# Kernel optimization log

Hardware: AMD Instinct MI355X
Metric: run time of the kernel (lower is better)

## Reference

```python
import jax, jax.numpy as jnp
import numpy as np

B, T, H = 32, 2000, 512      # batch, encoder frames, d_model
L = 256                      # max label length (padded output tokens)
THRESHOLD = 0.95


def setup_inputs() -> dict:
    key = jax.random.key(0)
    k1, k2, k3 = jax.random.split(key, 3)
    hidden = jax.random.normal(k1, (B, T, H), dtype=jnp.float32)
    alphas = jax.random.uniform(k2, (B, T), dtype=jnp.float32)
    target_lengths = jax.random.randint(k3, (B,), 64, L + 1)
    return {"hidden": hidden, "alphas": alphas, "target_lengths": target_lengths}


def _cif(hidden, alphas):
    # Continuous integrate-and-fire scan over time.
    Bt, Tt, Ht = hidden.shape

    def step(carry, xs):
        integrate, frame = carry          # [B], [B,H]
        alpha, h = xs                     # [B], [B,H]
        dist_completion = 1.0 - integrate
        integrate = integrate + alpha
        fire = integrate >= THRESHOLD     # [B] bool
        cur = jnp.where(fire, dist_completion, alpha)
        remainds = alpha - cur
        frame_out = frame + cur[:, None] * h
        integ_next = jnp.where(fire, integrate - 1.0, integrate)
        frame_next = jnp.where(fire[:, None], remainds[:, None] * h, frame_out)
        return (integ_next, frame_next), (frame_out, fire)

    init = (jnp.zeros((Bt,), hidden.dtype), jnp.zeros((Bt, Ht), hidden.dtype))
    _, (frames, fires) = jax.lax.scan(step, init, (alphas.T, jnp.swapaxes(hidden, 0, 1)))
    frames = jnp.swapaxes(frames, 0, 1)   # [B,T,H] accumulated frame at each step
    fires = fires.T                        # [B,T] fire events

    # Gather fired frames into padded [B, L, H] token tensor (vectorized scatter).
    tok = jnp.cumsum(fires.astype(jnp.int32), axis=1) - 1   # token index per fired frame
    valid = fires & (tok >= 0) & (tok < L)
    out = jnp.zeros((Bt, L, Ht), hidden.dtype)
    b_idx = jnp.arange(Bt)[:, None]
    out = out.at[b_idx, jnp.clip(tok, 0, L - 1)].add(
        frames * valid[..., None].astype(hidden.dtype))
    return out


def reference(hidden, alphas, target_lengths):
    # Rescale alphas so each row sums to target length (noise term omitted).
    num = target_lengths.astype(alphas.dtype)
    alphas = alphas * (num / alphas.sum(-1))[:, None]
    return _cif(hidden, alphas)
```

## Files before the change

kernel.cpp:

```cpp
#include <hip/hip_runtime.h>

#define BB 32
#define TT 2000
#define NG 500
#define NW 63
#define HH 512
#define LL 256
#define THRESH 0.95f


__global__ __launch_bounds__(256) void cif_scan_kernel(
    const float* __restrict__ alphas, const int* __restrict__ tlen,
    int2* __restrict__ rec, int* __restrict__ nfires,
    float* __restrict__ scale_g)
{
    const int b = blockIdx.x;
    const int tid = threadIdx.x;
    __shared__ float sa[TT];
    __shared__ float sinteg[TT];
    __shared__ double red[256];
    __shared__ unsigned smask[NW];
    __shared__ int spre[NW + 1];
    __shared__ float s_scale;

    const float4* a4 = (const float4*)(alphas + b * TT);
    float4* sa4 = (float4*)sa;
    double s = 0.0;
    for (int g = tid; g < NG; g += 256) {
        float4 v = a4[g];
        sa4[g] = v;
        s += (double)v.x + (double)v.y + (double)v.z + (double)v.w;
    }
    red[tid] = s;
    __syncthreads();
    for (int off = 128; off > 0; off >>= 1) {
        if (tid < off) red[tid] += red[tid + off];
        __syncthreads();
    }
    if (tid == 0) {
        const float sumf = (float)red[0];
        const float sc = (float)tlen[b] / sumf;
        s_scale = sc;
        scale_g[b] = sc;
    }
    __syncthreads();
    const float sc = s_scale;

    for (int g = tid; g < NG; g += 256) {
        float4 v = sa4[g];
        v.x *= sc; v.y *= sc; v.z *= sc; v.w *= sc;
        sa4[g] = v;
    }
    __syncthreads();

    if (tid == 0) {
        const float4* s4 = (const float4*)sa;
        float4* ip4 = (float4*)sinteg;
        float integ = 0.0f;
        unsigned mask = 0;
        float4 buf[8];
        #pragma unroll
        for (int i = 0; i < 8; ++i) buf[i] = s4[i];

        for (int w = 0; w < 62; ++w) {
            #pragma unroll
            for (int i = 0; i < 8; ++i) {
                const int g = w * 8 + i;
                const float4 c = buf[i];
                if (g + 8 < NG) buf[i] = s4[g + 8];
                const float av[4] = {c.x, c.y, c.z, c.w};
                float iv[4];
                #pragma unroll
                for (int j = 0; j < 4; ++j) {
                    const float a = av[j];
                    float ii = integ + a;
                    const bool fire = (ii >= THRESH);
                    const float iim1 = ii - 1.0f;
                    ii = fire ? iim1 : ii;
                    mask |= fire ? (1u << (i * 4 + j)) : 0u;
                    iv[j] = ii;
                    integ = ii;
                }
                ip4[g] = make_float4(iv[0], iv[1], iv[2], iv[3]);
            }
            smask[w] = mask;
            mask = 0;
        }
        #pragma unroll
        for (int i = 0; i < 4; ++i) {
            const int g = 496 + i;
            const float4 c = buf[i];
            const float av[4] = {c.x, c.y, c.z, c.w};
            float iv[4];
            #pragma unroll
            for (int j = 0; j < 4; ++j) {
                const float a = av[j];
                float ii = integ + a;
                const bool fire = (ii >= THRESH);
                const float iim1 = ii - 1.0f;
                ii = fire ? iim1 : ii;
                mask |= fire ? (1u << (i * 4 + j)) : 0u;
                iv[j] = ii;
                integ = ii;
            }
            ip4[g] = make_float4(iv[0], iv[1], iv[2], iv[3]);
        }
        smask[62] = mask;
    }
    __syncthreads();

    if (tid == 0) {
        int r = 0;
        for (int w = 0; w < NW; ++w) { spre[w] = r; r += __popc(smask[w]); }
        spre[NW] = r;
        nfires[b] = (r < LL) ? r : LL;
    }
    __syncthreads();
    if (tid < NW) {
        unsigned m = smask[tid];
        int tok = spre[tid];
        while (m) {
            const int j = __ffs(m) - 1;
            m &= m - 1;
            const int t = tid * 32 + j;
            if (tok < LL) {
                const float dist = (t == 0) ? 1.0f : (1.0f - sinteg[t - 1]);
                int2 r; r.x = t; r.y = __float_as_int(dist);
                rec[b * LL + tok] = r;
            }
            ++tok;
        }
    }
}

__global__ __launch_bounds__(128) void cif_gather_kernel(
    const float* __restrict__ hidden, const float* __restrict__ alphas,
    const float* __restrict__ scale_g, const int2* __restrict__ rec,
    const int* __restrict__ nfires, float* __restrict__ out)
{
    const int l = blockIdx.x;
    const int b = blockIdx.y;
    const int tid = threadIdx.x;

    float4 acc = make_float4(0.f, 0.f, 0.f, 0.f);
    const int F = nfires[b];
    if (l < F) {
        const int2 re = rec[b * LL + l];
        const int e = re.x;
        const float dist = __int_as_float(re.y);
        const float sc = scale_g[b];
        const float* hb = hidden + (size_t)b * TT * HH + (size_t)tid * 4;
        const float* ab = alphas + b * TT;
        int t0 = 0;
        if (l > 0) {
            const int2 rp = rec[b * LL + l - 1];
            const int sp = rp.x;
            const float dp = __int_as_float(rp.y);
            const float rem = ab[sp] * sc - dp;
            const float4 hv = *(const float4*)(hb + (size_t)sp * HH);
            acc.x = rem * hv.x; acc.y = rem * hv.y;
            acc.z = rem * hv.z; acc.w = rem * hv.w;
            t0 = sp + 1;
        }
        int t = t0;
        float w0 = (t < e) ? ab[t] * sc : dist;
        float4 h0 = *(const float4*)(hb + (size_t)t * HH);
        if (t < e) {
            float w1 = (t + 1 < e) ? ab[t + 1] * sc : dist;
            float4 h1 = *(const float4*)(hb + (size_t)(t + 1) * HH);
            while (t + 2 <= e) {
                const float w2 = (t + 2 < e) ? ab[t + 2] * sc : dist;
                const float4 h2 = *(const float4*)(hb + (size_t)(t + 2) * HH);
                acc.x += w0 * h0.x; acc.y += w0 * h0.y;
                acc.z += w0 * h0.z; acc.w += w0 * h0.w;
                w0 = w1; h0 = h1; w1 = w2; h1 = h2; ++t;
            }
            acc.x += w0 * h0.x; acc.y += w0 * h0.y;
            acc.z += w0 * h0.z; acc.w += w0 * h0.w;
            w0 = w1; h0 = h1;
        }
        acc.x += w0 * h0.x; acc.y += w0 * h0.y;
        acc.z += w0 * h0.z; acc.w += w0 * h0.w;
    }
    *(float4*)(out + ((size_t)b * LL + l) * HH + (size_t)tid * 4) = acc;
}

extern "C" void kernel_launch(void* const* d_in, const int* in_sizes, int n_in,
                              void* d_out, int out_size, void* d_ws, size_t ws_size,
                              hipStream_t stream) {
    const float* hidden = (const float*)d_in[0];
    const float* alphas = (const float*)d_in[1];
    const int*   tlen   = (const int*)d_in[2];
    float* out = (float*)d_out;

    int2*  rec     = (int2*)d_ws;
    int*   nfires  = (int*)(rec + BB * LL);
    float* scale_g = (float*)(nfires + BB);

    cif_scan_kernel<<<BB, 256, 0, stream>>>(alphas, tlen, rec, nfires, scale_g);
    cif_gather_kernel<<<dim3(LL, BB), 128, 0, stream>>>(hidden, alphas, scale_g,
                                                        rec, nfires, out);
}
```

Measured before the change: 264.6 us.

## Split scale reduction and batch eight rows per scan block with chunked transposed staging

Moves the alpha-sum reduction into its own kernel and turns the scan into 4 blocks, each handling 8 batch rows. Each block streams alphas in 512-frame chunks into a padded transposed shared buffer, and 8 threads scan their rows in parallel. Firing records are emitted serially per row with a carried token counter. This lowers the scan's block count and adds an extra launch, trading occupancy for shared staging. The serial per-thread record emission may lengthen the critical path.

```diff
diff --git a/kernel.cpp b/kernel.cpp
--- a/kernel.cpp
+++ b/kernel.cpp
@@ -3,32 +3,28 @@
 #define BB 32
 #define TT 2000
 #define NG 500
-#define NW 63
 #define HH 512
 #define LL 256
 #define THRESH 0.95f
 
+#define CHUNK 512
+#define NCH 4
+#define BPB 8
+#define SPAD 9
+#define NWIN 16
 
-__global__ __launch_bounds__(256) void cif_scan_kernel(
+
+__global__ __launch_bounds__(256) void cif_scale_kernel(
     const float* __restrict__ alphas, const int* __restrict__ tlen,
-    int2* __restrict__ rec, int* __restrict__ nfires,
     float* __restrict__ scale_g)
 {
     const int b = blockIdx.x;
     const int tid = threadIdx.x;
-    __shared__ float sa[TT];
-    __shared__ float sinteg[TT];
     __shared__ double red[256];
-    __shared__ unsigned smask[NW];
-    __shared__ int spre[NW + 1];
-    __shared__ float s_scale;
-
     const float4* a4 = (const float4*)(alphas + b * TT);
-    float4* sa4 = (float4*)sa;
     double s = 0.0;
     for (int g = tid; g < NG; g += 256) {
         float4 v = a4[g];
-        sa4[g] = v;
         s += (double)v.x + (double)v.y + (double)v.z + (double)v.w;
     }
     red[tid] = s;
@@ -37,100 +33,88 @@
         if (tid < off) red[tid] += red[tid + off];
         __syncthreads();
     }
-    if (tid == 0) {
-        const float sumf = (float)red[0];
-        const float sc = (float)tlen[b] / sumf;
-        s_scale = sc;
-        scale_g[b] = sc;
-    }
-    __syncthreads();
-    const float sc = s_scale;
+    if (tid == 0)
+        scale_g[b] = (float)tlen[b] / (float)red[0];
+}
 
-    for (int g = tid; g < NG; g += 256) {
-        float4 v = sa4[g];
-        v.x *= sc; v.y *= sc; v.z *= sc; v.w *= sc;
-        sa4[g] = v;
-    }
+__global__ __launch_bounds__(256) void cif_scan_kernel(
+    const float* __restrict__ alphas, const float* __restrict__ scale_g,
+    int2* __restrict__ rec, int* __restrict__ nfires)
+{
+    const int b0 = blockIdx.x * BPB;
+    const int tid = threadIdx.x;
+    __shared__ float saT[CHUNK * SPAD];
+    __shared__ float ipT[CHUNK * SPAD];
+    __shared__ unsigned smask[NWIN * BPB];
+    __shared__ float scs[BPB];
+
+    if (tid < BPB) scs[tid] = scale_g[b0 + tid];
     __syncthreads();
 
-    if (tid == 0) {
-        const float4* s4 = (const float4*)sa;
-        float4* ip4 = (float4*)sinteg;
-        float integ = 0.0f;
-        unsigned mask = 0;
-        float4 buf[8];
-        #pragma unroll
-        for (int i = 0; i < 8; ++i) buf[i] = s4[i];
+    float integ = 0.0f;
+    float carry_in = 0.0f;
+    int tok = 0;
 
-        for (int w = 0; w < 62; ++w) {
+    for (int c = 0; c < NCH; ++c) {
+        {
+            const int bl = tid >> 5;
+            const int lane = tid & 31;
+            const float sc = scs[bl];
+            const float* arow = alphas + (size_t)(b0 + bl) * TT + c * CHUNK;
             #pragma unroll
-            for (int i = 0; i < 8; ++i) {
-                const int g = w * 8 + i;
-                const float4 c = buf[i];
-                if (g + 8 < NG) buf[i] = s4[g + 8];
-                const float av[4] = {c.x, c.y, c.z, c.w};
-                float iv[4];
+            for (int j = 0; j < CHUNK / 32; ++j) {
+                const int t = lane + j * 32;
+                const int gt = c * CHUNK + t;
+                const float a = (gt < TT) ? arow[t] : 0.0f;
+                saT[t * SPAD + bl] = a * sc;
+            }
+        }
+        __syncthreads();
+
+        if (tid < BPB) {
+            carry_in = integ;
+            for (int w = 0; w < NWIN; ++w) {
+                unsigned mask = 0;
                 #pragma unroll
-                for (int j = 0; j < 4; ++j) {
-                    const float a = av[j];
+                for (int j = 0; j < 32; ++j) {
+                    const int t = w * 32 + j;
+                    const float a = saT[t * SPAD + tid];
                     float ii = integ + a;
                     const bool fire = (ii >= THRESH);
                     const float iim1 = ii - 1.0f;
                     ii = fire ? iim1 : ii;
-                    mask |= fire ? (1u << (i * 4 + j)) : 0u;
-                    iv[j] = ii;
+                    mask |= fire ? (1u << j) : 0u;
+                    ipT[t * SPAD + tid] = ii;
                     integ = ii;
                 }
-                ip4[g] = make_float4(iv[0], iv[1], iv[2], iv[3]);
+                smask[w * BPB + tid] = mask;
             }
-            smask[w] = mask;
-            mask = 0;
         }
-        #pragma unroll
-        for (int i = 0; i < 4; ++i) {
-            const int g = 496 + i;
-            const float4 c = buf[i];
-            const float av[4] = {c.x, c.y, c.z, c.w};
-            float iv[4];
-            #pragma unroll
-            for (int j = 0; j < 4; ++j) {
-                const float a = av[j];
-                float ii = integ + a;
-                const bool fire = (ii >= THRESH);
-                const float iim1 = ii - 1.0f;
-                ii = fire ? iim1 : ii;
-                mask |= fire ? (1u << (i * 4 + j)) : 0u;
-                iv[j] = ii;
-                integ = ii;
+        __syncthreads();
+
+        if (tid < BPB) {
+            const int b = b0 + tid;
+            for (int w = 0; w < NWIN; ++w) {
+                unsigned m = smask[w * BPB + tid];
+                while (m) {
+                    const int j = __ffs(m) - 1;
+                    m &= m - 1;
+                    const int t = w * 32 + j;
+                    if (tok < LL) {
+                        const float prev = (t == 0) ? carry_in
+                                                    : ipT[(t - 1) * SPAD + tid];
+                        int2 r;
+                        r.x = c * CHUNK + t;
+                        r.y = __float_as_int(1.0f - prev);
+                        rec[b * LL + tok] = r;
+                    }
+                    ++tok;
+                }
             }
-            ip4[g] = make_float4(iv[0], iv[1], iv[2], iv[3]);
         }
-        smask[62] = mask;
+        __syncthreads();
     }
-    __syncthreads();
-
-    if (tid == 0) {
-        int r = 0;
-        for (int w = 0; w < NW; ++w) { spre[w] = r; r += __popc(smask[w]); }
-        spre[NW] = r;
-        nfires[b] = (r < LL) ? r : LL;
-    }
-    __syncthreads();
-    if (tid < NW) {
-        unsigned m = smask[tid];
-        int tok = spre[tid];
-        while (m) {
-            const int j = __ffs(m) - 1;
-            m &= m - 1;
-            const int t = tid * 32 + j;
-            if (tok < LL) {
-                const float dist = (t == 0) ? 1.0f : (1.0f - sinteg[t - 1]);
-                int2 r; r.x = t; r.y = __float_as_int(dist);
-                rec[b * LL + tok] = r;
-            }
-            ++tok;
-        }
-    }
+    if (tid < BPB) nfires[b0 + tid] = (tok < LL) ? tok : LL;
 }
 
 __global__ __launch_bounds__(128) void cif_gather_kernel(
@@ -197,7 +181,8 @@
     int*   nfires  = (int*)(rec + BB * LL);
     float* scale_g = (float*)(nfires + BB);
 
-    cif_scan_kernel<<<BB, 256, 0, stream>>>(alphas, tlen, rec, nfires, scale_g);
+    cif_scale_kernel<<<BB, 256, 0, stream>>>(alphas, tlen, scale_g);
+    cif_scan_kernel<<<4, 256, 0, stream>>>(alphas, scale_g, rec, nfires);
     cif_gather_kernel<<<dim3(LL, BB), 128, 0, stream>>>(hidden, alphas, scale_g,
                                                         rec, nfires, out);
 }
```

Measured after the change: 284.9 us. 7.7% more time.
